# Optimization experiments

Hardware: AMD Instinct MI355X
Metric: run time of the kernel (lower is better)

The kernel has to match this reference:

```python
import jax, jax.numpy as jnp
import numpy as np

B, S, D = 2, 2048, 2048
KVH, QPG, HD = 8, 4, 64          # kv heads, q heads per group, head size
THETA = 1024.0
PARTIAL = 0.5
SOFT_CAP = 50.0
EPS = 1e-5


def setup_inputs() -> dict:
    key = jax.random.key(0)
    ks = jax.random.split(key, 8)
    scale = 0.02
    return {
        "x": jax.random.normal(ks[0], (B, S, D), jnp.float32),
        "wq": jax.random.normal(ks[1], (KVH, QPG, HD, D), jnp.float32) * scale,
        "wk": jax.random.normal(ks[2], (KVH, HD, D), jnp.float32) * scale,
        "wv": jax.random.normal(ks[3], (KVH, HD, D), jnp.float32) * scale,
        "wo": jax.random.normal(ks[4], (D, KVH, QPG, HD), jnp.float32) * scale,
        "qn_w": jnp.ones((HD,), jnp.float32),
        "kn_w": jnp.ones((HD,), jnp.float32),
        "pos_ids": jnp.arange(S, dtype=jnp.int32),
    }


def _rms_norm(t, w):
    var = jnp.mean(jnp.square(t), axis=-1, keepdims=True)
    return t * jax.lax.rsqrt(var + EPS) * w


def _rope_tables(pos_ids):
    half = HD // 2
    rotated_size = int(HD * PARTIAL)
    inv_freq = 1.0 / THETA ** (jnp.arange(0, 2 * half, 2, dtype=jnp.float32) / rotated_size)
    inv_freq = jnp.where(jnp.arange(half) < rotated_size // 2, inv_freq, 0.0)
    freqs = pos_ids.astype(jnp.float32)[:, None] * inv_freq[None, :]   # [S, half]
    emb = jnp.concatenate([freqs, freqs], axis=-1)                      # [S, HD]
    return jnp.cos(emb), jnp.sin(emb)


def _apply_rope(t, cos, sin):
    # t: [..., S, HD]; rotate_half: (x1, x2) -> (-x2, x1)
    half = HD // 2
    x1, x2 = t[..., :half], t[..., half:]
    rot = jnp.concatenate([-x2, x1], axis=-1)
    return t * cos + rot * sin


def reference(x, wq, wk, wv, wo, qn_w, kn_w, pos_ids):
    # QKV projections (GQA)
    q = jnp.einsum("bsd,gphd->bgpsh", x, wq)   # [B,KVH,QPG,S,HD]
    k = jnp.einsum("bsd,ghd->bgsh", x, wk)      # [B,KVH,S,HD]
    v = jnp.einsum("bsd,ghd->bgsh", x, wv)

    # QK-norm (RMS over head dim)
    q = _rms_norm(q, qn_w)
    k = _rms_norm(k, kn_w)

    # partial RoPE
    cos, sin = _rope_tables(pos_ids)            # [S, HD]
    q = _apply_rope(q, cos, sin).astype(x.dtype)
    k = _apply_rope(k, cos, sin).astype(x.dtype)

    # attention in fp32 (upcast_attn) with soft cap and causal mask
    scale = 1.0 / jnp.sqrt(jnp.float32(HD))
    scores = jnp.einsum("bgpsh,bgth->bgpst", q.astype(jnp.float32), k.astype(jnp.float32)) * scale
    scores = SOFT_CAP * jnp.tanh(scores / SOFT_CAP)
    causal = pos_ids[:, None] >= pos_ids[None, :]                    # [S, S]
    scores = jnp.where(causal, scores, jnp.finfo(jnp.float32).min)
    probs = jax.nn.softmax(scores, axis=-1)
    attn = jnp.einsum("bgpst,bgth->bgpsh", probs, v.astype(jnp.float32)).astype(x.dtype)

    # output projection (flatten kv_head x q_heads_per_group -> heads)
    out = jnp.einsum("bgpsh,dgph->bsd", attn, wo)
    return out
```

## Files before the change

kernel.cpp:

```cpp
#include <hip/hip_runtime.h>
#include <stdint.h>

#define S_LEN   2048
#define D_MODEL 2048
#define N_KVH   8
#define N_QPG   4
#define N_HD    64

typedef __attribute__((ext_vector_type(8))) short  short8;
typedef __attribute__((ext_vector_type(4))) short  short4v;
typedef __attribute__((ext_vector_type(4))) float  float4v;

__device__ __forceinline__ unsigned short f2bf(float x) {
    unsigned int u = __float_as_uint(x);
    u = (u + 0x7fffu + ((u >> 16) & 1u)) >> 16;
    return (unsigned short)u;
}

__device__ __forceinline__ void gload_lds16(const unsigned short* g, unsigned short* l) {
    __builtin_amdgcn_global_load_lds((const __attribute__((address_space(1))) unsigned int*)g,
                                     (__attribute__((address_space(3))) unsigned int*)l,
                                     16, 0, 0);
}

__device__ __forceinline__ short8 lds_read8(const unsigned short* p) {
    union { short8 s8; short4v s4[2]; } u;
    u.s4[0] = *(const short4v*)p;
    u.s4[1] = *(const short4v*)(p + 4);
    return u.s8;
}

__global__ __launch_bounds__(256) void cvt_all(const float* __restrict__ x,
                                               const float* __restrict__ wq,
                                               const float* __restrict__ wk,
                                               const float* __restrict__ wv,
                                               const float* __restrict__ wo,
                                               unsigned short* __restrict__ xb,
                                               unsigned short* __restrict__ wqb,
                                               unsigned short* __restrict__ wkb,
                                               unsigned short* __restrict__ wvb,
                                               unsigned short* __restrict__ wob) {
    size_t i = (size_t)blockIdx.x * 256 + threadIdx.x;
    const float* src; unsigned short* dst; size_t off;
    if      (i < 1048576) { src = x;  dst = xb;  off = i; }
    else if (i < 1572864) { src = wq; dst = wqb; off = i - 1048576; }
    else if (i < 1703936) { src = wk; dst = wkb; off = i - 1572864; }
    else if (i < 1835008) { src = wv; dst = wvb; off = i - 1703936; }
    else                  { src = wo; dst = wob; off = i - 1835008; }
    const float4* p = (const float4*)src + off * 2;
    float4 a = p[0], b = p[1];
    union { unsigned short us[8]; uint4 v; } u;
    u.us[0] = f2bf(a.x); u.us[1] = f2bf(a.y); u.us[2] = f2bf(a.z); u.us[3] = f2bf(a.w);
    u.us[4] = f2bf(b.x); u.us[5] = f2bf(b.y); u.us[6] = f2bf(b.z); u.us[7] = f2bf(b.w);
    ((uint4*)dst)[off] = u.v;
}

__global__ __launch_bounds__(256)
void gemm_qkv(const unsigned short* __restrict__ xb,
              const unsigned short* __restrict__ wqb,
              const unsigned short* __restrict__ wkb,
              const unsigned short* __restrict__ wvb,
              unsigned short* __restrict__ qout,
              unsigned short* __restrict__ kout,
              unsigned short* __restrict__ vtout,
              const float* __restrict__ qnw,
              const float* __restrict__ knw)
{
    __shared__ __align__(16) unsigned short Alds[128 * 32];
    __shared__ __align__(16) unsigned short Blds[128 * 32];

    const int tid  = threadIdx.x;
    const int lane = tid & 63;
    const int wave = tid >> 6;
    const int quad = lane >> 4;
    const int l15  = lane & 15;
    const int bx = blockIdx.x, by = blockIdx.y;
    const int role = (by < 16) ? 0 : (by < 20 ? 1 : 2);
    const unsigned short* A;
    const unsigned short* B;
    int m0, n0;
    if (role == 0)      { A = xb;  B = wqb; m0 = bx * 128; n0 = by * 128; }
    else if (role == 1) { A = xb;  B = wkb; m0 = bx * 128; n0 = (by - 16) * 128; }
    else                { A = wvb; B = xb;  m0 = (by - 20) * 128; n0 = bx * 128; }
    const int K = 2048;
    const int wm = (wave >> 1) * 64;
    const int wn = (wave & 1) * 64;

    float4v acc[4][4];
#pragma unroll
    for (int i = 0; i < 4; i++)
#pragma unroll
        for (int j = 0; j < 4; j++) acc[i][j] = (float4v){0.f, 0.f, 0.f, 0.f};

    const int j0 = wave * 2;
    const int lr = lane >> 2;
    const int lc = (lane & 3) * 8;
    const unsigned short* Ag = A + (size_t)(m0 + j0 * 16 + lr) * K + lc;
    const unsigned short* Bg = B + (size_t)(n0 + j0 * 16 + lr) * K + lc;
    unsigned short* Al = Alds + j0 * 512;
    unsigned short* Bl = Blds + j0 * 512;

    for (int k0 = 0; k0 < K; k0 += 32) {
        __syncthreads();
        gload_lds16(Ag + k0,          Al);
        gload_lds16(Ag + 16 * K + k0, Al + 512);
        gload_lds16(Bg + k0,          Bl);
        gload_lds16(Bg + 16 * K + k0, Bl + 512);
        __syncthreads();

        short8 af[4], bf[4];
#pragma unroll
        for (int mt = 0; mt < 4; mt++)
            af[mt] = *(const short8*)(Alds + (wm + mt * 16 + l15) * 32 + quad * 8);
#pragma unroll
        for (int nt = 0; nt < 4; nt++)
            bf[nt] = *(const short8*)(Blds + (wn + nt * 16 + l15) * 32 + quad * 8);
#pragma unroll
        for (int mt = 0; mt < 4; mt++)
#pragma unroll
            for (int nt = 0; nt < 4; nt++)
                acc[mt][nt] = __builtin_amdgcn_mfma_f32_16x16x32_bf16(af[mt], bf[nt], acc[mt][nt], 0, 0, 0);
    }

    const int nb = n0 + wn;
    const float* nw = (role == 1) ? knw : qnw;
#pragma unroll
    for (int mt = 0; mt < 4; mt++) {
#pragma unroll
        for (int r = 0; r < 4; r++) {
            const int m = m0 + wm + mt * 16 + quad * 4 + r;
            if (role == 2) {
#pragma unroll
                for (int nt = 0; nt < 4; nt++) {
                    int n = nb + nt * 16 + l15;
                    vtout[((size_t)(n >> 11) * 512 + m) * 2048 + (n & 2047)] =
                        f2bf(acc[mt][nt][r]);
                }
            } else {
                float v0 = acc[mt][0][r], v1 = acc[mt][1][r], v2 = acc[mt][2][r], v3 = acc[mt][3][r];
                float s2 = v0 * v0 + v1 * v1 + v2 * v2 + v3 * v3;
#pragma unroll
                for (int off = 1; off < 16; off <<= 1) s2 += __shfl_xor(s2, off, 64);
                float rs = rsqrtf(s2 * (1.0f / 64.0f) + 1e-5f);
                float nv0 = v0 * rs * nw[0 * 16 + l15];
                float nv1 = v1 * rs * nw[1 * 16 + l15];
                float nv2 = v2 * rs * nw[2 * 16 + l15];
                float nv3 = v3 * rs * nw[3 * 16 + l15];
                const int bidx = m >> 11, s = m & 2047;
                float ang = (float)s * exp2f(-0.625f * (float)l15);
                float sn, cs;
                __sincosf(ang, &sn, &cs);
                float o0 = nv0 * cs - nv2 * sn;
                float o2 = nv2 * cs + nv0 * sn;
                unsigned short* dst;
                if (role == 0) {
                    const int g = nb >> 8, p = (nb >> 6) & 3;
                    dst = qout + ((((size_t)bidx * N_KVH + g) * N_QPG + p) * S_LEN + s) * N_HD;
                } else {
                    const int g = nb >> 6;
                    dst = kout + (((size_t)bidx * N_KVH + g) * S_LEN + s) * N_HD;
                }
                dst[0 * 16 + l15] = f2bf(o0);
                dst[1 * 16 + l15] = f2bf(nv1);
                dst[2 * 16 + l15] = f2bf(o2);
                dst[3 * 16 + l15] = f2bf(nv3);
            }
        }
    }
}

__global__ __launch_bounds__(256)
void gemm_out(const unsigned short* __restrict__ A,
              const unsigned short* __restrict__ B,
              float* __restrict__ C,
              int M, int N, int K)
{
    __shared__ __align__(16) unsigned short Alds[128 * 32];
    __shared__ __align__(16) unsigned short Blds[128 * 32];

    const int tid  = threadIdx.x;
    const int lane = tid & 63;
    const int wave = tid >> 6;
    const int quad = lane >> 4;
    const int l15  = lane & 15;
    const int m0 = blockIdx.x * 128;
    const int n0 = blockIdx.y * 128;
    const int wm = (wave >> 1) * 64;
    const int wn = (wave & 1) * 64;

    float4v acc[4][4];
#pragma unroll
    for (int i = 0; i < 4; i++)
#pragma unroll
        for (int j = 0; j < 4; j++) acc[i][j] = (float4v){0.f, 0.f, 0.f, 0.f};

    const int j0 = wave * 2;
    const int lr = lane >> 2;
    const int lc = (lane & 3) * 8;
    const unsigned short* Ag = A + (size_t)(m0 + j0 * 16 + lr) * K + lc;
    const unsigned short* Bg = B + (size_t)(n0 + j0 * 16 + lr) * K + lc;
    unsigned short* Al = Alds + j0 * 512;
    unsigned short* Bl = Blds + j0 * 512;

    for (int k0 = 0; k0 < K; k0 += 32) {
        __syncthreads();
        gload_lds16(Ag + k0,          Al);
        gload_lds16(Ag + 16 * K + k0, Al + 512);
        gload_lds16(Bg + k0,          Bl);
        gload_lds16(Bg + 16 * K + k0, Bl + 512);
        __syncthreads();

        short8 af[4], bf[4];
#pragma unroll
        for (int mt = 0; mt < 4; mt++)
            af[mt] = *(const short8*)(Alds + (wm + mt * 16 + l15) * 32 + quad * 8);
#pragma unroll
        for (int nt = 0; nt < 4; nt++)
            bf[nt] = *(const short8*)(Blds + (wn + nt * 16 + l15) * 32 + quad * 8);
#pragma unroll
        for (int mt = 0; mt < 4; mt++)
#pragma unroll
            for (int nt = 0; nt < 4; nt++)
                acc[mt][nt] = __builtin_amdgcn_mfma_f32_16x16x32_bf16(af[mt], bf[nt], acc[mt][nt], 0, 0, 0);
    }

    const int nb = n0 + wn;
#pragma unroll
    for (int mt = 0; mt < 4; mt++) {
#pragma unroll
        for (int r = 0; r < 4; r++) {
            const int m = m0 + wm + mt * 16 + quad * 4 + r;
#pragma unroll
            for (int nt = 0; nt < 4; nt++) {
                int n = nb + nt * 16 + l15;
                C[(size_t)m * N + n] = acc[mt][nt][r];
            }
        }
    }
}

#define PSTRIDE 68

__global__ __launch_bounds__(256)
void attn_kernel(const unsigned short* __restrict__ Q,
                 const unsigned short* __restrict__ Kb,
                 const unsigned short* __restrict__ Vt,
                 unsigned short* __restrict__ O)
{
    __shared__ __align__(16) unsigned short Plds[4 * 32 * PSTRIDE];

    const int tid  = threadIdx.x;
    const int lane = tid & 63;
    const int w    = tid >> 6;
    const int quad = lane >> 4;
    const int l15  = lane & 15;
    const int qx = blockIdx.y;
    const int bg = blockIdx.x;
    const int b = bg >> 3, g = bg & 7;

    const unsigned short* qbase  = Q  + (((size_t)b * N_KVH + g) * N_QPG + w) * S_LEN * N_HD;
    const unsigned short* kbase  = Kb + ((size_t)b * N_KVH + g) * S_LEN * N_HD;
    const unsigned short* vtbase = Vt + ((size_t)b * N_KVH + g) * (size_t)N_HD * S_LEN;

    unsigned short* Pw = Plds + w * (32 * PSTRIDE);

    for (int half = 0; half < 2; half++) {
        const int qt = half ? (63 - qx) : qx;
        const int qrow0 = qt * 32;

        short8 qf[2][2];
#pragma unroll
        for (int mt = 0; mt < 2; mt++)
#pragma unroll
            for (int ks = 0; ks < 2; ks++)
                qf[mt][ks] = *(const short8*)(qbase + (size_t)(qrow0 + mt * 16 + l15) * N_HD + ks * 32 + quad * 8);

        float4v o_acc[2][4];
#pragma unroll
        for (int mt = 0; mt < 2; mt++)
#pragma unroll
            for (int nt = 0; nt < 4; nt++) o_acc[mt][nt] = (float4v){0.f, 0.f, 0.f, 0.f};
        float rsum[2][4];
#pragma unroll
        for (int mt = 0; mt < 2; mt++)
#pragma unroll
            for (int r = 0; r < 4; r++) rsum[mt][r] = 0.f;

        const int ktend = qrow0 >> 6;

        short8 kf[4][2];
#pragma unroll
        for (int nt = 0; nt < 4; nt++)
#pragma unroll
            for (int ks = 0; ks < 2; ks++)
                kf[nt][ks] = *(const short8*)(kbase + (size_t)(nt * 16 + l15) * N_HD + ks * 32 + quad * 8);

        for (int kt = 0; kt <= ktend; kt++) {
            float4v s_acc[2][4];
#pragma unroll
            for (int mt = 0; mt < 2; mt++)
#pragma unroll
                for (int nt = 0; nt < 4; nt++) s_acc[mt][nt] = (float4v){0.f, 0.f, 0.f, 0.f};
            __builtin_amdgcn_s_setprio(1);
#pragma unroll
            for (int ks = 0; ks < 2; ks++)
#pragma unroll
                for (int mt = 0; mt < 2; mt++)
#pragma unroll
                    for (int nt = 0; nt < 4; nt++)
                        s_acc[mt][nt] = __builtin_amdgcn_mfma_f32_16x16x32_bf16(qf[mt][ks], kf[nt][ks], s_acc[mt][nt], 0, 0, 0);
            __builtin_amdgcn_s_setprio(0);

            short8 vf[4][2];
#pragma unroll
            for (int nt = 0; nt < 4; nt++)
#pragma unroll
                for (int ks = 0; ks < 2; ks++)
                    vf[nt][ks] = *(const short8*)(vtbase + (size_t)(nt * 16 + l15) * S_LEN + kt * 64 + ks * 32 + quad * 8);

            if (kt < ktend) {
#pragma unroll
                for (int nt = 0; nt < 4; nt++)
#pragma unroll
                    for (int ks = 0; ks < 2; ks++)
                        kf[nt][ks] = *(const short8*)(kbase + (size_t)((kt + 1) * 64 + nt * 16 + l15) * N_HD + ks * 32 + quad * 8);
            }

            const bool diag = (kt == ktend);
#pragma unroll
            for (int mt = 0; mt < 2; mt++) {
#pragma unroll
                for (int r = 0; r < 4; r++) {
                    const int s_q  = qrow0 + mt * 16 + quad * 4 + r;
                    const int prow = (mt * 16 + quad * 4 + r) * PSTRIDE;
#pragma unroll
                    for (int nt = 0; nt < 4; nt++) {
                        float a = s_acc[mt][nt][r];
                        float u = a * a;
                        float wv = fmaf(u, -3.757018e-7f, 0.18033688f);
                        float p = __builtin_amdgcn_exp2f(fmaf(a, wv, -72.13475204f));
                        if (diag) {
                            int s_k = kt * 64 + nt * 16 + l15;
                            p = (s_k <= s_q) ? p : 0.0f;
                        }
                        rsum[mt][r] += p;
                        Pw[prow + nt * 16 + l15] =
                            (unsigned short)((__float_as_uint(p) + 0x8000u) >> 16);
                    }
                }
            }

#pragma unroll
            for (int ks = 0; ks < 2; ks++) {
                short8 pf[2];
#pragma unroll
                for (int mt = 0; mt < 2; mt++)
                    pf[mt] = lds_read8(Pw + (mt * 16 + l15) * PSTRIDE + ks * 32 + quad * 8);
                __builtin_amdgcn_s_setprio(1);
#pragma unroll
                for (int mt = 0; mt < 2; mt++)
#pragma unroll
                    for (int nt = 0; nt < 4; nt++)
                        o_acc[mt][nt] = __builtin_amdgcn_mfma_f32_16x16x32_bf16(pf[mt], vf[nt][ks], o_acc[mt][nt], 0, 0, 0);
                __builtin_amdgcn_s_setprio(0);
            }
        }

#pragma unroll
        for (int mt = 0; mt < 2; mt++) {
#pragma unroll
            for (int r = 0; r < 4; r++) {
                float s = rsum[mt][r];
                s += __shfl_xor(s, 1, 64);
                s += __shfl_xor(s, 2, 64);
                s += __shfl_xor(s, 4, 64);
                s += __shfl_xor(s, 8, 64);
                float inv = 1.0f / s;
                int s_q = qrow0 + mt * 16 + quad * 4 + r;
                size_t rowoff = ((size_t)(b * S_LEN + s_q)) * D_MODEL + (g * N_QPG + w) * N_HD;
#pragma unroll
                for (int nt = 0; nt < 4; nt++)
                    O[rowoff + nt * 16 + l15] = f2bf(o_acc[mt][nt][r] * inv);
            }
        }
    }
}

extern "C" void kernel_launch(void* const* d_in, const int* in_sizes, int n_in,
                              void* d_out, int out_size, void* d_ws, size_t ws_size,
                              hipStream_t stream)
{
    const float* x    = (const float*)d_in[0];
    const float* wq   = (const float*)d_in[1];
    const float* wk   = (const float*)d_in[2];
    const float* wv   = (const float*)d_in[3];
    const float* wo   = (const float*)d_in[4];
    const float* qn_w = (const float*)d_in[5];
    const float* kn_w = (const float*)d_in[6];

    char* ws = (char*)d_ws;
    unsigned short* xb  = (unsigned short*)(ws + 0);
    unsigned short* wqb = (unsigned short*)(ws + 16777216);
    unsigned short* wkb = (unsigned short*)(ws + 25165824);
    unsigned short* wvb = (unsigned short*)(ws + 27262976);
    unsigned short* wob = (unsigned short*)(ws + 29360128);
    unsigned short* qb  = (unsigned short*)(ws + 37748736);
    unsigned short* kb  = (unsigned short*)(ws + 54525952);
    unsigned short* vt  = (unsigned short*)(ws + 58720256);
    unsigned short* ab  = (unsigned short*)(ws + 62914560);

    cvt_all<<<dim3(9216), 256, 0, stream>>>(x, wq, wk, wv, wo, xb, wqb, wkb, wvb, wob);

    gemm_qkv<<<dim3(32, 24), 256, 0, stream>>>(xb, wqb, wkb, wvb, qb, kb, vt, qn_w, kn_w);

    attn_kernel<<<dim3(16, 32), 256, 0, stream>>>(qb, kb, vt, ab);

    gemm_out<<<dim3(32, 16), 256, 0, stream>>>(ab, wob, (float*)d_out, 4096, 2048, 2048);
}
```

Measured before the change: 385.7 us.

## Double-buffer LDS tiles in QKV and output GEMMs to overlap loads with MFMA

Both the QKV projection GEMM and the output projection GEMM now keep two LDS buffers for the A and B tiles. The global-to-LDS load for the next k-slice is issued before the MFMAs on the current slice, and the loop steps by 64 with one barrier per half-step. This is meant to hide global load latency behind matrix math, at the cost of twice the LDS per block, which may reduce occupancy.

```diff
diff --git a/kernel.cpp b/kernel.cpp
--- a/kernel.cpp
+++ b/kernel.cpp
@@ -55,6 +55,29 @@
     ((uint4*)dst)[off] = u.v;
 }
 
+#define GSTAGE(AL, BL, KO)                         \
+    gload_lds16(Ag + (KO),          (AL));         \
+    gload_lds16(Ag + 16 * K + (KO), (AL) + 512);   \
+    gload_lds16(Bg + (KO),          (BL));         \
+    gload_lds16(Bg + 16 * K + (KO), (BL) + 512);
+
+#define GCOMPUTE(OFF)                                                          \
+    {                                                                          \
+        short8 af[4], bf[4];                                                   \
+        _Pragma("unroll")                                                      \
+        for (int mt = 0; mt < 4; mt++)                                         \
+            af[mt] = *(const short8*)(Alds + (OFF) + (wm + mt * 16 + l15) * 32 + quad * 8); \
+        _Pragma("unroll")                                                      \
+        for (int nt = 0; nt < 4; nt++)                                         \
+            bf[nt] = *(const short8*)(Blds + (OFF) + (wn + nt * 16 + l15) * 32 + quad * 8); \
+        _Pragma("unroll")                                                      \
+        for (int mt = 0; mt < 4; mt++)                                         \
+            _Pragma("unroll")                                                  \
+            for (int nt = 0; nt < 4; nt++)                                     \
+                acc[mt][nt] = __builtin_amdgcn_mfma_f32_16x16x32_bf16(         \
+                    af[mt], bf[nt], acc[mt][nt], 0, 0, 0);                     \
+    }
+
 __global__ __launch_bounds__(256)
 void gemm_qkv(const unsigned short* __restrict__ xb,
               const unsigned short* __restrict__ wqb,
@@ -66,8 +89,8 @@
               const float* __restrict__ qnw,
               const float* __restrict__ knw)
 {
-    __shared__ __align__(16) unsigned short Alds[128 * 32];
-    __shared__ __align__(16) unsigned short Blds[128 * 32];
+    __shared__ __align__(16) unsigned short Alds[2 * 128 * 32];
+    __shared__ __align__(16) unsigned short Blds[2 * 128 * 32];
 
     const int tid  = threadIdx.x;
     const int lane = tid & 63;
@@ -97,29 +120,21 @@
     const int lc = (lane & 3) * 8;
     const unsigned short* Ag = A + (size_t)(m0 + j0 * 16 + lr) * K + lc;
     const unsigned short* Bg = B + (size_t)(n0 + j0 * 16 + lr) * K + lc;
-    unsigned short* Al = Alds + j0 * 512;
-    unsigned short* Bl = Blds + j0 * 512;
-
-    for (int k0 = 0; k0 < K; k0 += 32) {
+    unsigned short* Al0 = Alds + j0 * 512;
+    unsigned short* Bl0 = Blds + j0 * 512;
+    unsigned short* Al1 = Alds + 4096 + j0 * 512;
+    unsigned short* Bl1 = Blds + 4096 + j0 * 512;
+
+    GSTAGE(Al0, Bl0, 0);
+    __syncthreads();
+
+    for (int k0 = 0; k0 < K; k0 += 64) {
+        GSTAGE(Al1, Bl1, k0 + 32);
+        GCOMPUTE(0);
         __syncthreads();
-        gload_lds16(Ag + k0,          Al);
-        gload_lds16(Ag + 16 * K + k0, Al + 512);
-        gload_lds16(Bg + k0,          Bl);
-        gload_lds16(Bg + 16 * K + k0, Bl + 512);
+        if (k0 + 64 < K) { GSTAGE(Al0, Bl0, k0 + 64); }
+        GCOMPUTE(4096);
         __syncthreads();
-
-        short8 af[4], bf[4];
-#pragma unroll
-        for (int mt = 0; mt < 4; mt++)
-            af[mt] = *(const short8*)(Alds + (wm + mt * 16 + l15) * 32 + quad * 8);
-#pragma unroll
-        for (int nt = 0; nt < 4; nt++)
-            bf[nt] = *(const short8*)(Blds + (wn + nt * 16 + l15) * 32 + quad * 8);
-#pragma unroll
-        for (int mt = 0; mt < 4; mt++)
-#pragma unroll
-            for (int nt = 0; nt < 4; nt++)
-                acc[mt][nt] = __builtin_amdgcn_mfma_f32_16x16x32_bf16(af[mt], bf[nt], acc[mt][nt], 0, 0, 0);
     }
 
     const int nb = n0 + wn;
@@ -175,8 +190,8 @@
               float* __restrict__ C,
               int M, int N, int K)
 {
-    __shared__ __align__(16) unsigned short Alds[128 * 32];
-    __shared__ __align__(16) unsigned short Blds[128 * 32];
+    __shared__ __align__(16) unsigned short Alds[2 * 128 * 32];
+    __shared__ __align__(16) unsigned short Blds[2 * 128 * 32];
 
     const int tid  = threadIdx.x;
     const int lane = tid & 63;
@@ -199,29 +214,21 @@
     const int lc = (lane & 3) * 8;
     const unsigned short* Ag = A + (size_t)(m0 + j0 * 16 + lr) * K + lc;
     const unsigned short* Bg = B + (size_t)(n0 + j0 * 16 + lr) * K + lc;
-    unsigned short* Al = Alds + j0 * 512;
-    unsigned short* Bl = Blds + j0 * 512;
-
-    for (int k0 = 0; k0 < K; k0 += 32) {
+    unsigned short* Al0 = Alds + j0 * 512;
+    unsigned short* Bl0 = Blds + j0 * 512;
+    unsigned short* Al1 = Alds + 4096 + j0 * 512;
+    unsigned short* Bl1 = Blds + 4096 + j0 * 512;
+
+    GSTAGE(Al0, Bl0, 0);
+    __syncthreads();
+
+    for (int k0 = 0; k0 < K; k0 += 64) {
+        GSTAGE(Al1, Bl1, k0 + 32);
+        GCOMPUTE(0);
         __syncthreads();
-        gload_lds16(Ag + k0,          Al);
-        gload_lds16(Ag + 16 * K + k0, Al + 512);
-        gload_lds16(Bg + k0,          Bl);
-        gload_lds16(Bg + 16 * K + k0, Bl + 512);
+        if (k0 + 64 < K) { GSTAGE(Al0, Bl0, k0 + 64); }
+        GCOMPUTE(4096);
         __syncthreads();
-
-        short8 af[4], bf[4];
-#pragma unroll
-        for (int mt = 0; mt < 4; mt++)
-            af[mt] = *(const short8*)(Alds + (wm + mt * 16 + l15) * 32 + quad * 8);
-#pragma unroll
-        for (int nt = 0; nt < 4; nt++)
-            bf[nt] = *(const short8*)(Blds + (wn + nt * 16 + l15) * 32 + quad * 8);
-#pragma unroll
-        for (int mt = 0; mt < 4; mt++)
-#pragma unroll
-            for (int nt = 0; nt < 4; nt++)
-                acc[mt][nt] = __builtin_amdgcn_mfma_f32_16x16x32_bf16(af[mt], bf[nt], acc[mt][nt], 0, 0, 0);
     }
 
     const int nb = n0 + wn;
```

Result: no change. 382.0 us (-1.0%).
